# Kernel tuning notes

Hardware: AMD Instinct MI355X
Metric: run time of the kernel (lower is better)

Reference implementation:

```python
import jax, jax.numpy as jnp
import numpy as np

NUM_FEATURES = 128   # conv spatial length
WINDOW = 128         # conv channels / lstm seq len
KC = 16              # kernels per group
KS = 3               # conv kernel size
FC1 = 32             # number of independent LSTMs
H = 32               # lstm hidden size
NL = 2               # lstm layers
PAD = 1
POOL_LEN = (NUM_FEATURES + 2 * PAD) // 2  # maxpool(k=2,s=2,p=1) output length
B = 128


def setup_inputs():
    key = jax.random.key(0)
    ks = jax.random.split(key, 13)
    x = jax.random.normal(ks[0], (B, WINDOW, NUM_FEATURES), jnp.float32)
    conv_w = jax.random.normal(ks[1], (WINDOW * KC, 1, KS), jnp.float32) * 0.3
    conv_b = jax.random.normal(ks[2], (WINDOW * KC,), jnp.float32) * 0.1
    fc1_in = KC * POOL_LEN
    fc1_w = jax.random.normal(ks[3], (FC1, fc1_in), jnp.float32) * 0.02
    fc1_b = jax.random.normal(ks[4], (FC1,), jnp.float32) * 0.02
    w_ih0 = jax.random.normal(ks[5], (FC1, 4 * H), jnp.float32) * 0.1          # layer0, input size 1
    w_ih1 = jax.random.normal(ks[6], (NL - 1, FC1, 4 * H, H), jnp.float32) * 0.1
    w_hh = jax.random.normal(ks[7], (NL, FC1, 4 * H, H), jnp.float32) * 0.1
    b_lstm = jax.random.normal(ks[8], (NL, FC1, 4 * H), jnp.float32) * 0.1     # bias_ih + bias_hh combined
    mu_w = jax.random.normal(ks[9], (1, FC1 * H), jnp.float32) * 0.05
    mu_b = jax.random.normal(ks[10], (1,), jnp.float32) * 0.05
    lv_w = jax.random.normal(ks[11], (1, FC1 * H), jnp.float32) * 0.05
    lv_b = jax.random.normal(ks[12], (1,), jnp.float32) * 0.05
    return {"x": x, "conv_w": conv_w, "conv_b": conv_b, "fc1_w": fc1_w, "fc1_b": fc1_b,
            "w_ih0": w_ih0, "w_ih1": w_ih1, "w_hh": w_hh, "b_lstm": b_lstm,
            "mu_w": mu_w, "mu_b": mu_b, "lv_w": lv_w, "lv_b": lv_b}


def _lstm_cell(gates, c_prev):
    # torch gate order: i, f, g, o
    i, f, g, o = jnp.split(gates, 4, axis=-1)
    c_new = jax.nn.sigmoid(f) * c_prev + jax.nn.sigmoid(i) * jnp.tanh(g)
    h_new = jax.nn.sigmoid(o) * jnp.tanh(c_new)
    return h_new, c_new


def reference(x, conv_w, conv_b, fc1_w, fc1_b, w_ih0, w_ih1, w_hh, b_lstm, mu_w, mu_b, lv_w, lv_b):
    bsz = x.shape[0]
    # grouped conv1d: groups = WINDOW, each group maps 1 -> KC channels
    y = jax.lax.conv_general_dilated(x, conv_w, window_strides=(1,), padding=[(PAD, PAD)],
                                     feature_group_count=WINDOW,
                                     dimension_numbers=('NCH', 'OIH', 'NCH'))
    y = jax.nn.relu(y + conv_b[None, :, None])
    neg = jnp.finfo(y.dtype).min
    y = jnp.pad(y, ((0, 0), (0, 0), (PAD, PAD)), constant_values=neg)
    y = y.reshape(bsz, WINDOW * KC, POOL_LEN, 2).max(axis=-1)
    # regroup to [B, WINDOW, KC*POOL_LEN] (channel layout = group-major, matches torch view)
    y = y.reshape(bsz, WINDOW, KC * POOL_LEN)
    z = jnp.einsum('bwi,oi->bwo', y, fc1_w) + fc1_b   # [B, WINDOW, FC1]

    # FC1 independent NL-layer LSTMs batched over the feature axis; time axis = WINDOW
    h0 = jnp.zeros((NL, bsz, FC1, H), z.dtype)
    c0 = jnp.zeros_like(h0)

    def step(carry, x_t):  # x_t: [B, FC1]
        h, c = carry
        hs, cs = [], []
        gates = jnp.einsum('bf,fg->bfg', x_t, w_ih0) + jnp.einsum('bfh,fgh->bfg', h[0], w_hh[0]) + b_lstm[0]
        h_l, c_l = _lstm_cell(gates, c[0])
        hs.append(h_l); cs.append(c_l)
        for l in range(1, NL):
            gates = (jnp.einsum('bfh,fgh->bfg', h_l, w_ih1[l - 1])
                     + jnp.einsum('bfh,fgh->bfg', h[l], w_hh[l]) + b_lstm[l])
            h_l, c_l = _lstm_cell(gates, c[l])
            hs.append(h_l); cs.append(c_l)
        return (jnp.stack(hs), jnp.stack(cs)), None

    (h_fin, _), _ = jax.lax.scan(step, (h0, c0), jnp.transpose(z, (1, 0, 2)))
    combined = h_fin[-1].reshape(bsz, FC1 * H)  # top layer, last step; feature-major like torch.cat
    mu = combined @ mu_w.T + mu_b
    log_var = combined @ lv_w.T + lv_b
    sigma = jnp.exp(0.5 * log_var)
    return (mu - 1.96 * sigma, mu, mu + 1.96 * sigma, log_var)
```

## Files before the change

kernel.cpp:

```cpp
#include <hip/hip_runtime.h>
#include <hip/hip_bf16.h>
#include <math.h>

#define BATCH 128
#define WIN   128
#define NF    128
#define KC    16
#define POOL  65
#define NFC1  32
#define HS    32
#define LW    40
#define KP    1056
#define PSTR  1064

typedef float f32x4 __attribute__((ext_vector_type(4)));
typedef short bf16x8 __attribute__((ext_vector_type(8)));

__device__ __forceinline__ float cellf(float& c, float gi, float gf, float gg, float go) {
    float ei = __expf(-gi);
    float eg = __expf(2.f * gg);
    float ef = __expf(-gf);
    float sf = __builtin_amdgcn_rcpf(1.f + ef);
    float num = eg - 1.f;
    float den = (1.f + ei) * (eg + 1.f);
    c = fmaf(sf, c, num * __builtin_amdgcn_rcpf(den));
    float cc = fminf(fmaxf(c, -30.f), 30.f);
    float eo = __expf(-go);
    float ec = __expf(2.f * cc);
    return (ec - 1.f) * __builtin_amdgcn_rcpf((1.f + eo) * (ec + 1.f));
}
__device__ __forceinline__ unsigned short f2bf(float x) {
    __hip_bfloat16 h = __float2bfloat16(x);
    unsigned short u; __builtin_memcpy(&u, &h, 2); return u;
}
__device__ __forceinline__ float bf2f(unsigned short u) {
    unsigned int v = ((unsigned int)u) << 16;
    float f; __builtin_memcpy(&f, &v, 4); return f;
}
__device__ __forceinline__ bf16x8 load_row8_bf16(const float* row) {
    float4 lo = ((const float4*)row)[0];
    float4 hi = ((const float4*)row)[1];
    union { bf16x8 v; unsigned short u[8]; } t;
    t.u[0] = f2bf(lo.x); t.u[1] = f2bf(lo.y); t.u[2] = f2bf(lo.z); t.u[3] = f2bf(lo.w);
    t.u[4] = f2bf(hi.x); t.u[5] = f2bf(hi.y); t.u[6] = f2bf(hi.z); t.u[7] = f2bf(hi.w);
    return t.v;
}

__global__ __launch_bounds__(256) void k0_wconv(
    const float* __restrict__ fc1_w, unsigned short* __restrict__ w_bf)
{
    const int o = blockIdx.x;
    for (int i = threadIdx.x; i < KP; i += 256) {
        float v = (i < KC * POOL) ? fc1_w[(size_t)o * (KC * POOL) + i] : 0.f;
        w_bf[(size_t)o * KP + i] = f2bf(v);
    }
}

__global__ __launch_bounds__(128, 2) void k1_conv_fc1(
    const float* __restrict__ x, const float* __restrict__ conv_w, const float* __restrict__ conv_b,
    const unsigned short* __restrict__ w_bf, const float* __restrict__ fc1_b, float* __restrict__ z)
{
    __shared__ __align__(16) unsigned short xp[16][132];
    __shared__ __align__(16) unsigned short poolb[16 * PSTR];
    __shared__ float cw[KC][3];
    __shared__ float cb[KC];
    __shared__ float fb[NFC1];

    const int w = blockIdx.x >> 3;
    const int bbase = (blockIdx.x & 7) * 16;
    const int tid = threadIdx.x;

    if (tid < KC * 3) cw[tid / 3][tid % 3] = conv_w[(w * KC + tid / 3) * 3 + tid % 3];
    if (tid >= 64 && tid < 64 + KC) cb[tid - 64] = conv_b[w * KC + (tid - 64)];
    if (tid >= 96 && tid < 96 + NFC1) fb[tid - 96] = fc1_b[tid - 96];

    for (int i = tid; i < 16 * 132; i += 128) {
        int b = i / 132, p = i % 132;
        float v = (p >= 1 && p <= NF) ? x[(size_t)(bbase + b) * (WIN * NF) + (size_t)w * NF + (p - 1)] : 0.f;
        xp[b][p] = f2bf(v);
    }
    __syncthreads();

    {
        const int b0 = tid >> 4;
        const int k = tid & 15;
        const float w0 = cw[k][0], w1 = cw[k][1], w2 = cw[k][2], bb = cb[k];
        #pragma unroll
        for (int half = 0; half < 2; ++half) {
            const int b = b0 + half * 8;
            float v1 = 0.f;
            float v2 = bf2f(xp[b][0]);
            float v3 = bf2f(xp[b][1]);
            unsigned short* prow = &poolb[b * PSTR + k * POOL];
            #pragma unroll 1
            for (int j = 0; j < POOL; ++j) {
                float v0 = v1; v1 = v2; v2 = v3;
                v3 = bf2f(xp[b][2 * j + 2]);
                float oa = bb + w0 * v0 + w1 * v1 + w2 * v2;
                float ob = bb + w0 * v1 + w1 * v2 + w2 * v3;
                float m = 0.f;
                if (j > 0)        m = fmaxf(m, oa);
                if (j < POOL - 1) m = fmaxf(m, ob);
                prow[j] = f2bf(m);
            }
        }
    }
    for (int i = tid; i < 16 * (KP - KC * POOL); i += 128) {
        int b = i >> 4, c = i & 15;
        poolb[b * PSTR + KC * POOL + c] = 0;
    }
    __syncthreads();

    const int lane = tid & 63;
    const int wid = tid >> 6;
    const int col = lane & 15;
    const int kg = lane >> 4;
    const int g = wid * 16 + col;
    f32x4 acc;
    {
        float bias = fb[g];
        acc[0] = bias; acc[1] = bias; acc[2] = bias; acc[3] = bias;
    }
    const unsigned short* wrow = w_bf + (size_t)g * KP;
    #pragma unroll 4
    for (int ks = 0; ks < KP / 32; ++ks) {
        bf16x8 aP = *(const bf16x8*)&poolb[col * PSTR + ks * 32 + kg * 8];
        bf16x8 bW = *(const bf16x8*)&wrow[ks * 32 + kg * 8];
        acc = __builtin_amdgcn_mfma_f32_16x16x32_bf16(aP, bW, acc, 0, 0, 0);
    }
    float4 st; st.x = acc[0]; st.y = acc[1]; st.z = acc[2]; st.w = acc[3];
    *(float4*)&z[(size_t)w * (NFC1 * BATCH) + (size_t)g * BATCH + bbase + kg * 4] = st;
}

__global__ __launch_bounds__(256, 1) void k2_lstm_mfma(
    const float* __restrict__ w_ih0, const float* __restrict__ w_ih1,
    const float* __restrict__ w_hh, const float* __restrict__ b_lstm,
    const float* __restrict__ z, float* __restrict__ h1fin)
{
    __shared__ float zs[WIN][16];
    __shared__ __align__(16) unsigned short h0b[2][16 * LW];
    __shared__ __align__(16) unsigned short h1b[2][16 * LW];

    const int f = blockIdx.x >> 3;
    const int bbase = (blockIdx.x & 7) * 16;
    const int tid = threadIdx.x;
    const int wid = tid >> 6, lane = tid & 63;
    const bool isL0 = (wid < 2);
    const int s = wid & 1;
    const int col = lane & 15;
    const int kg = lane >> 4;

    for (int i = tid; i < WIN * 16; i += 256) {
        int t = i >> 4, c = i & 15;
        zs[t][c] = z[(size_t)t * (NFC1 * BATCH) + f * BATCH + bbase + c];
    }
    for (int i = tid; i < 2 * 16 * LW; i += 256) { h0b[0][i] = 0; h1b[0][i] = 0; }

    const float* WA = isL0 ? (w_hh + (size_t)f * 4096)
                           : (w_ih1 + (size_t)f * 4096);
    const float* WV = w_hh + (size_t)(NFC1 + f) * 4096;
    bf16x8 fA[4], fB[4];
    float bias[4], wi0[4];
    const int loff = isL0 ? 0 : (NFC1 * 128);
    #pragma unroll
    for (int gi = 0; gi < 4; ++gi) {
        int nt = gi * 2 + s;
        int g = nt * 16 + col;
        fA[gi] = load_row8_bf16(WA + g * 32 + kg * 8);
        if (!isL0) fB[gi] = load_row8_bf16(WV + g * 32 + kg * 8);
        bias[gi] = b_lstm[loff + f * 128 + g];
        wi0[gi] = w_ih0[f * 128 + g];
    }
    __syncthreads();

    const int hread = col * LW + kg * 8;
    float cst[4] = {0.f, 0.f, 0.f, 0.f};
    int p = 0;
    f32x4 zv = *(const f32x4*)&zs[0][kg * 4];

    #pragma unroll 1
    for (int it = 0; it <= WIN; ++it) {
        const bool doL0 = isL0 && (it < WIN);
        const bool doL1 = (!isL0) && (it >= 1);

        if (doL0) {
            bf16x8 hA = *(const bf16x8*)&h0b[p][hread];
            f32x4 aI, aF, aG, aO;
            #pragma unroll
            for (int j = 0; j < 4; ++j) {
                aI[j] = fmaf(zv[j], wi0[0], bias[0]);
                aF[j] = fmaf(zv[j], wi0[1], bias[1]);
                aG[j] = fmaf(zv[j], wi0[2], bias[2]);
                aO[j] = fmaf(zv[j], wi0[3], bias[3]);
            }
            aI = __builtin_amdgcn_mfma_f32_16x16x32_bf16(hA, fA[0], aI, 0, 0, 0);
            aF = __builtin_amdgcn_mfma_f32_16x16x32_bf16(hA, fA[1], aF, 0, 0, 0);
            aG = __builtin_amdgcn_mfma_f32_16x16x32_bf16(hA, fA[2], aG, 0, 0, 0);
            aO = __builtin_amdgcn_mfma_f32_16x16x32_bf16(hA, fA[3], aO, 0, 0, 0);
            if (it + 1 < WIN) zv = *(const f32x4*)&zs[it + 1][kg * 4];
            #pragma unroll
            for (int j = 0; j < 4; ++j) {
                float h = cellf(cst[j], aI[j], aF[j], aG[j], aO[j]);
                h0b[p ^ 1][(kg * 4 + j) * LW + 16 * s + col] = f2bf(h);
            }
        }
        if (doL1) {
            bf16x8 hA = *(const bf16x8*)&h0b[p][hread];
            bf16x8 hB = *(const bf16x8*)&h1b[p][hread];
            f32x4 aI, aF, aG, aO;
            #pragma unroll
            for (int j = 0; j < 4; ++j) { aI[j] = bias[0]; aF[j] = bias[1]; aG[j] = bias[2]; aO[j] = bias[3]; }
            aI = __builtin_amdgcn_mfma_f32_16x16x32_bf16(hA, fA[0], aI, 0, 0, 0);
            aI = __builtin_amdgcn_mfma_f32_16x16x32_bf16(hB, fB[0], aI, 0, 0, 0);
            aF = __builtin_amdgcn_mfma_f32_16x16x32_bf16(hA, fA[1], aF, 0, 0, 0);
            aF = __builtin_amdgcn_mfma_f32_16x16x32_bf16(hB, fB[1], aF, 0, 0, 0);
            aG = __builtin_amdgcn_mfma_f32_16x16x32_bf16(hA, fA[2], aG, 0, 0, 0);
            aG = __builtin_amdgcn_mfma_f32_16x16x32_bf16(hB, fB[2], aG, 0, 0, 0);
            aO = __builtin_amdgcn_mfma_f32_16x16x32_bf16(hA, fA[3], aO, 0, 0, 0);
            aO = __builtin_amdgcn_mfma_f32_16x16x32_bf16(hB, fB[3], aO, 0, 0, 0);
            if (it < WIN) {
                #pragma unroll
                for (int j = 0; j < 4; ++j) {
                    float h = cellf(cst[j], aI[j], aF[j], aG[j], aO[j]);
                    h1b[p ^ 1][(kg * 4 + j) * LW + 16 * s + col] = f2bf(h);
                }
            } else {
                #pragma unroll
                for (int j = 0; j < 4; ++j) {
                    float h = cellf(cst[j], aI[j], aF[j], aG[j], aO[j]);
                    h1fin[(size_t)(bbase + kg * 4 + j) * (NFC1 * HS) + f * HS + 16 * s + col] = h;
                }
            }
        }
        __syncthreads();
        p ^= 1;
    }
}

__global__ __launch_bounds__(128) void k3_head(
    const float* __restrict__ h1fin, const float* __restrict__ mu_w, const float* __restrict__ mu_b,
    const float* __restrict__ lv_w, const float* __restrict__ lv_b, float* __restrict__ out)
{
    const int b = blockIdx.x, tid = threadIdx.x;
    const float* hrow = h1fin + (size_t)b * (NFC1 * HS);
    float am = 0.f, al = 0.f;
    for (int i = tid; i < NFC1 * HS; i += 128) {
        float h = hrow[i];
        am = fmaf(h, mu_w[i], am);
        al = fmaf(h, lv_w[i], al);
    }
    for (int off = 32; off >= 1; off >>= 1) {
        am += __shfl_down(am, off, 64);
        al += __shfl_down(al, off, 64);
    }
    __shared__ float sm[2], sl[2];
    const int wv = tid >> 6, ln = tid & 63;
    if (ln == 0) { sm[wv] = am; sl[wv] = al; }
    __syncthreads();
    if (tid == 0) {
        float mu = sm[0] + sm[1] + mu_b[0];
        float lv = sl[0] + sl[1] + lv_b[0];
        float sg = expf(0.5f * lv);
        out[b]           = mu - 1.96f * sg;
        out[128 + b]     = mu;
        out[256 + b]     = mu + 1.96f * sg;
        out[384 + b]     = lv;
    }
}

extern "C" void kernel_launch(void* const* d_in, const int* in_sizes, int n_in,
                              void* d_out, int out_size, void* d_ws, size_t ws_size,
                              hipStream_t stream)
{
    const float* x      = (const float*)d_in[0];
    const float* conv_w = (const float*)d_in[1];
    const float* conv_b = (const float*)d_in[2];
    const float* fc1_w  = (const float*)d_in[3];
    const float* fc1_b  = (const float*)d_in[4];
    const float* w_ih0  = (const float*)d_in[5];
    const float* w_ih1  = (const float*)d_in[6];
    const float* w_hh   = (const float*)d_in[7];
    const float* b_lstm = (const float*)d_in[8];
    const float* mu_w   = (const float*)d_in[9];
    const float* mu_b   = (const float*)d_in[10];
    const float* lv_w   = (const float*)d_in[11];
    const float* lv_b   = (const float*)d_in[12];
    float* out = (float*)d_out;

    float* z     = (float*)d_ws;
    float* h1fin = z + (size_t)WIN * NFC1 * BATCH;
    unsigned short* w_bf = (unsigned short*)(h1fin + (size_t)BATCH * NFC1 * HS);

    k0_wconv<<<dim3(NFC1), dim3(256), 0, stream>>>(fc1_w, w_bf);
    k1_conv_fc1<<<dim3(WIN * 8), dim3(128), 0, stream>>>(x, conv_w, conv_b, w_bf, fc1_b, z);
    k2_lstm_mfma<<<dim3(NFC1 * 8), dim3(256), 0, stream>>>(w_ih0, w_ih1, w_hh, b_lstm, z, h1fin);
    k3_head<<<dim3(BATCH), dim3(128), 0, stream>>>(h1fin, mu_w, mu_b, lv_w, lv_b, out);
}
```

Before: 100.4 us.

## Fold exp2 scaling into LSTM weights, unroll ping-pong, vectorize conv/z loads

Pre-scales the LSTM gate weights, biases and input weights by -log2e or 2*log2e so the gate activations can use raw exp2 without negation or multiplies, and clamps with fmed3. The recurrent loop is unrolled by two with static ping-pong shared buffers, which removes the buffer-index arithmetic. The x and z staging loads become float4 vector loads, and the conv pooling loop is partially unrolled. Scaling the weights before the bf16 conversion slightly changes rounding.

```diff
diff --git a/kernel.cpp b/kernel.cpp
--- a/kernel.cpp
+++ b/kernel.cpp
@@ -16,17 +16,17 @@
 typedef float f32x4 __attribute__((ext_vector_type(4)));
 typedef short bf16x8 __attribute__((ext_vector_type(8)));
 
+#define LOG2E   1.442695041f
+#define LOG2E2  2.885390082f
+
 __device__ __forceinline__ float cellf(float& c, float gi, float gf, float gg, float go) {
-    float ei = __expf(-gi);
-    float eg = __expf(2.f * gg);
-    float ef = __expf(-gf);
+    float ei = __builtin_amdgcn_exp2f(gi);
+    float ef = __builtin_amdgcn_exp2f(gf);
+    float eg = __builtin_amdgcn_exp2f(gg);
+    float eo = __builtin_amdgcn_exp2f(go);
     float sf = __builtin_amdgcn_rcpf(1.f + ef);
-    float num = eg - 1.f;
-    float den = (1.f + ei) * (eg + 1.f);
-    c = fmaf(sf, c, num * __builtin_amdgcn_rcpf(den));
-    float cc = fminf(fmaxf(c, -30.f), 30.f);
-    float eo = __expf(-go);
-    float ec = __expf(2.f * cc);
+    c = fmaf(sf, c, (eg - 1.f) * __builtin_amdgcn_rcpf((1.f + ei) * (eg + 1.f)));
+    float ec = __builtin_amdgcn_exp2f(__builtin_amdgcn_fmed3f(c, -30.f, 30.f) * LOG2E2);
     return (ec - 1.f) * __builtin_amdgcn_rcpf((1.f + eo) * (ec + 1.f));
 }
 __device__ __forceinline__ unsigned short f2bf(float x) {
@@ -37,12 +37,12 @@
     unsigned int v = ((unsigned int)u) << 16;
     float f; __builtin_memcpy(&f, &v, 4); return f;
 }
-__device__ __forceinline__ bf16x8 load_row8_bf16(const float* row) {
+__device__ __forceinline__ bf16x8 load_row8_scaled(const float* row, float sc) {
     float4 lo = ((const float4*)row)[0];
     float4 hi = ((const float4*)row)[1];
     union { bf16x8 v; unsigned short u[8]; } t;
-    t.u[0] = f2bf(lo.x); t.u[1] = f2bf(lo.y); t.u[2] = f2bf(lo.z); t.u[3] = f2bf(lo.w);
-    t.u[4] = f2bf(hi.x); t.u[5] = f2bf(hi.y); t.u[6] = f2bf(hi.z); t.u[7] = f2bf(hi.w);
+    t.u[0] = f2bf(lo.x * sc); t.u[1] = f2bf(lo.y * sc); t.u[2] = f2bf(lo.z * sc); t.u[3] = f2bf(lo.w * sc);
+    t.u[4] = f2bf(hi.x * sc); t.u[5] = f2bf(hi.y * sc); t.u[6] = f2bf(hi.z * sc); t.u[7] = f2bf(hi.w * sc);
     return t.v;
 }
 
@@ -74,11 +74,13 @@
     if (tid >= 64 && tid < 64 + KC) cb[tid - 64] = conv_b[w * KC + (tid - 64)];
     if (tid >= 96 && tid < 96 + NFC1) fb[tid - 96] = fc1_b[tid - 96];
 
-    for (int i = tid; i < 16 * 132; i += 128) {
-        int b = i / 132, p = i % 132;
-        float v = (p >= 1 && p <= NF) ? x[(size_t)(bbase + b) * (WIN * NF) + (size_t)w * NF + (p - 1)] : 0.f;
-        xp[b][p] = f2bf(v);
-    }
+    for (int i = tid; i < 16 * 32; i += 128) {
+        int b = i >> 5, q = i & 31;
+        float4 v = ((const float4*)(x + (size_t)(bbase + b) * (WIN * NF) + (size_t)w * NF))[q];
+        unsigned short* dst = &xp[b][1 + q * 4];
+        dst[0] = f2bf(v.x); dst[1] = f2bf(v.y); dst[2] = f2bf(v.z); dst[3] = f2bf(v.w);
+    }
+    if (tid < 16) { xp[tid][0] = 0; xp[tid][129] = 0; xp[tid][130] = 0; xp[tid][131] = 0; }
     __syncthreads();
 
     {
@@ -92,7 +94,7 @@
             float v2 = bf2f(xp[b][0]);
             float v3 = bf2f(xp[b][1]);
             unsigned short* prow = &poolb[b * PSTR + k * POOL];
-            #pragma unroll 1
+            #pragma unroll 5
             for (int j = 0; j < POOL; ++j) {
                 float v0 = v1; v1 = v2; v2 = v3;
                 v3 = bf2f(xp[b][2 * j + 2]);
@@ -138,8 +140,10 @@
     const float* __restrict__ z, float* __restrict__ h1fin)
 {
     __shared__ float zs[WIN][16];
-    __shared__ __align__(16) unsigned short h0b[2][16 * LW];
-    __shared__ __align__(16) unsigned short h1b[2][16 * LW];
+    __shared__ __align__(16) unsigned short h0b0[16 * LW];
+    __shared__ __align__(16) unsigned short h0b1[16 * LW];
+    __shared__ __align__(16) unsigned short h1b0[16 * LW];
+    __shared__ __align__(16) unsigned short h1b1[16 * LW];
 
     const int f = blockIdx.x >> 3;
     const int bbase = (blockIdx.x & 7) * 16;
@@ -150,11 +154,15 @@
     const int col = lane & 15;
     const int kg = lane >> 4;
 
-    for (int i = tid; i < WIN * 16; i += 256) {
-        int t = i >> 4, c = i & 15;
-        zs[t][c] = z[(size_t)t * (NFC1 * BATCH) + f * BATCH + bbase + c];
-    }
-    for (int i = tid; i < 2 * 16 * LW; i += 256) { h0b[0][i] = 0; h1b[0][i] = 0; }
+    for (int i = tid; i < WIN * 4; i += 256) {
+        int t = i >> 2, q = i & 3;
+        ((float4*)&zs[t][0])[q] = ((const float4*)&z[(size_t)t * (NFC1 * BATCH) + f * BATCH + bbase])[q];
+    }
+    for (int i = tid; i < 16 * LW; i += 256) {
+        h0b0[i] = 0; h0b1[i] = 0; h1b0[i] = 0; h1b1[i] = 0;
+    }
+
+    const float gsc[4] = { -LOG2E, -LOG2E, LOG2E2, -LOG2E };
 
     const float* WA = isL0 ? (w_hh + (size_t)f * 4096)
                            : (w_ih1 + (size_t)f * 4096);
@@ -166,74 +174,82 @@
     for (int gi = 0; gi < 4; ++gi) {
         int nt = gi * 2 + s;
         int g = nt * 16 + col;
-        fA[gi] = load_row8_bf16(WA + g * 32 + kg * 8);
-        if (!isL0) fB[gi] = load_row8_bf16(WV + g * 32 + kg * 8);
-        bias[gi] = b_lstm[loff + f * 128 + g];
-        wi0[gi] = w_ih0[f * 128 + g];
+        fA[gi] = load_row8_scaled(WA + g * 32 + kg * 8, gsc[gi]);
+        if (!isL0) fB[gi] = load_row8_scaled(WV + g * 32 + kg * 8, gsc[gi]);
+        bias[gi] = b_lstm[loff + f * 128 + g] * gsc[gi];
+        wi0[gi] = w_ih0[f * 128 + g] * gsc[gi];
     }
     __syncthreads();
 
     const int hread = col * LW + kg * 8;
+    const int hw0 = (kg * 4 + 0) * LW + 16 * s + col;
     float cst[4] = {0.f, 0.f, 0.f, 0.f};
-    int p = 0;
     f32x4 zv = *(const f32x4*)&zs[0][kg * 4];
 
-    #pragma unroll 1
-    for (int it = 0; it <= WIN; ++it) {
-        const bool doL0 = isL0 && (it < WIN);
-        const bool doL1 = (!isL0) && (it >= 1);
-
-        if (doL0) {
-            bf16x8 hA = *(const bf16x8*)&h0b[p][hread];
-            f32x4 aI, aF, aG, aO;
-            #pragma unroll
-            for (int j = 0; j < 4; ++j) {
-                aI[j] = fmaf(zv[j], wi0[0], bias[0]);
-                aF[j] = fmaf(zv[j], wi0[1], bias[1]);
-                aG[j] = fmaf(zv[j], wi0[2], bias[2]);
-                aO[j] = fmaf(zv[j], wi0[3], bias[3]);
-            }
-            aI = __builtin_amdgcn_mfma_f32_16x16x32_bf16(hA, fA[0], aI, 0, 0, 0);
-            aF = __builtin_amdgcn_mfma_f32_16x16x32_bf16(hA, fA[1], aF, 0, 0, 0);
-            aG = __builtin_amdgcn_mfma_f32_16x16x32_bf16(hA, fA[2], aG, 0, 0, 0);
-            aO = __builtin_amdgcn_mfma_f32_16x16x32_bf16(hA, fA[3], aO, 0, 0, 0);
-            if (it + 1 < WIN) zv = *(const f32x4*)&zs[it + 1][kg * 4];
-            #pragma unroll
-            for (int j = 0; j < 4; ++j) {
-                float h = cellf(cst[j], aI[j], aF[j], aG[j], aO[j]);
-                h0b[p ^ 1][(kg * 4 + j) * LW + 16 * s + col] = f2bf(h);
-            }
-        }
-        if (doL1) {
-            bf16x8 hA = *(const bf16x8*)&h0b[p][hread];
-            bf16x8 hB = *(const bf16x8*)&h1b[p][hread];
-            f32x4 aI, aF, aG, aO;
-            #pragma unroll
-            for (int j = 0; j < 4; ++j) { aI[j] = bias[0]; aF[j] = bias[1]; aG[j] = bias[2]; aO[j] = bias[3]; }
-            aI = __builtin_amdgcn_mfma_f32_16x16x32_bf16(hA, fA[0], aI, 0, 0, 0);
-            aI = __builtin_amdgcn_mfma_f32_16x16x32_bf16(hB, fB[0], aI, 0, 0, 0);
-            aF = __builtin_amdgcn_mfma_f32_16x16x32_bf16(hA, fA[1], aF, 0, 0, 0);
-            aF = __builtin_amdgcn_mfma_f32_16x16x32_bf16(hB, fB[1], aF, 0, 0, 0);
-            aG = __builtin_amdgcn_mfma_f32_16x16x32_bf16(hA, fA[2], aG, 0, 0, 0);
-            aG = __builtin_amdgcn_mfma_f32_16x16x32_bf16(hB, fB[2], aG, 0, 0, 0);
-            aO = __builtin_amdgcn_mfma_f32_16x16x32_bf16(hA, fA[3], aO, 0, 0, 0);
-            aO = __builtin_amdgcn_mfma_f32_16x16x32_bf16(hB, fB[3], aO, 0, 0, 0);
+    auto body = [&](int it, const unsigned short* h0r, unsigned short* h0w,
+                            const unsigned short* h1r, unsigned short* h1w) {
+        if (isL0) {
             if (it < WIN) {
+                bf16x8 hA = *(const bf16x8*)&h0r[hread];
+                f32x4 aI, aF, aG, aO;
+                #pragma unroll
+                for (int j = 0; j < 4; ++j) {
+                    aI[j] = fmaf(zv[j], wi0[0], bias[0]);
+                    aF[j] = fmaf(zv[j], wi0[1], bias[1]);
+                    aG[j] = fmaf(zv[j], wi0[2], bias[2]);
+                    aO[j] = fmaf(zv[j], wi0[3], bias[3]);
+                }
+                aI = __builtin_amdgcn_mfma_f32_16x16x32_bf16(hA, fA[0], aI, 0, 0, 0);
+                aF = __builtin_amdgcn_mfma_f32_16x16x32_bf16(hA, fA[1], aF, 0, 0, 0);
+                aG = __builtin_amdgcn_mfma_f32_16x16x32_bf16(hA, fA[2], aG, 0, 0, 0);
+                aO = __builtin_amdgcn_mfma_f32_16x16x32_bf16(hA, fA[3], aO, 0, 0, 0);
+                if (it + 1 < WIN) zv = *(const f32x4*)&zs[it + 1][kg * 4];
                 #pragma unroll
                 for (int j = 0; j < 4; ++j) {
                     float h = cellf(cst[j], aI[j], aF[j], aG[j], aO[j]);
-                    h1b[p ^ 1][(kg * 4 + j) * LW + 16 * s + col] = f2bf(h);
+                    h0w[hw0 + j * LW] = f2bf(h);
                 }
-            } else {
+            }
+        } else {
+            if (it >= 1) {
+                bf16x8 hA = *(const bf16x8*)&h0r[hread];
+                bf16x8 hB = *(const bf16x8*)&h1r[hread];
+                f32x4 aI, aF, aG, aO;
                 #pragma unroll
-                for (int j = 0; j < 4; ++j) {
-                    float h = cellf(cst[j], aI[j], aF[j], aG[j], aO[j]);
-                    h1fin[(size_t)(bbase + kg * 4 + j) * (NFC1 * HS) + f * HS + 16 * s + col] = h;
+                for (int j = 0; j < 4; ++j) { aI[j] = bias[0]; aF[j] = bias[1]; aG[j] = bias[2]; aO[j] = bias[3]; }
+                aI = __builtin_amdgcn_mfma_f32_16x16x32_bf16(hA, fA[0], aI, 0, 0, 0);
+                aI = __builtin_amdgcn_mfma_f32_16x16x32_bf16(hB, fB[0], aI, 0, 0, 0);
+                aF = __builtin_amdgcn_mfma_f32_16x16x32_bf16(hA, fA[1], aF, 0, 0, 0);
+                aF = __builtin_amdgcn_mfma_f32_16x16x32_bf16(hB, fB[1], aF, 0, 0, 0);
+                aG = __builtin_amdgcn_mfma_f32_16x16x32_bf16(hA, fA[2], aG, 0, 0, 0);
+                aG = __builtin_amdgcn_mfma_f32_16x16x32_bf16(hB, fB[2], aG, 0, 0, 0);
+                aO = __builtin_amdgcn_mfma_f32_16x16x32_bf16(hA, fA[3], aO, 0, 0, 0);
+                aO = __builtin_amdgcn_mfma_f32_16x16x32_bf16(hB, fB[3], aO, 0, 0, 0);
+                if (it < WIN) {
+                    #pragma unroll
+                    for (int j = 0; j < 4; ++j) {
+                        float h = cellf(cst[j], aI[j], aF[j], aG[j], aO[j]);
+                        h1w[hw0 + j * LW] = f2bf(h);
+                    }
+                } else {
+                    #pragma unroll
+                    for (int j = 0; j < 4; ++j) {
+                        float h = cellf(cst[j], aI[j], aF[j], aG[j], aO[j]);
+                        h1fin[(size_t)(bbase + kg * 4 + j) * (NFC1 * HS) + f * HS + 16 * s + col] = h;
+                    }
                 }
             }
         }
+    };
+
+    body(0, h0b0, h0b1, h1b0, h1b1);
+    __syncthreads();
+    #pragma unroll 1
+    for (int it = 1; it <= WIN; it += 2) {
+        body(it,     h0b1, h0b0, h1b1, h1b0);
         __syncthreads();
-        p ^= 1;
+        body(it + 1, h0b0, h0b1, h1b0, h1b1);
+        __syncthreads();
     }
 }
 
```

New measurement: 86.44 us. -13.9%, faster.
